# Optimization experiments

Measured on AMD Instinct MI355X. Metric: run time of the kernel, lower is better.

Reference implementation:

```python
import jax, jax.numpy as jnp
import numpy as np

DIM = 1024
HEADS = 16
SCALE = DIM ** (-0.5)  # note: full dim, matching original module


def setup_inputs() -> dict:
    key = jax.random.key(0)
    k1, k2, k3, k4 = jax.random.split(key, 4)
    x = jax.random.normal(k1, (8, 1024, DIM), dtype=jnp.float32)
    w_qkv = jax.random.normal(k2, (DIM, 3 * DIM), dtype=jnp.float32) * (DIM ** -0.5)
    w_out = jax.random.normal(k3, (DIM, DIM), dtype=jnp.float32) * (DIM ** -0.5)
    b_out = jax.random.normal(k4, (DIM,), dtype=jnp.float32) * 0.01
    return {"x": x, "w_qkv": w_qkv, "w_out": w_out, "b_out": b_out}


def reference(x, w_qkv, w_out, b_out):
    b, n, dim = x.shape
    h = HEADS
    d = dim // h
    qkv = x @ w_qkv  # [b, n, 3*dim]
    q, k, v = jnp.split(qkv, 3, axis=-1)
    # 'b n (h d) -> b h n d'
    def to_heads(t):
        return t.reshape(b, n, h, d).transpose(0, 2, 1, 3)
    q, k, v = to_heads(q), to_heads(k), to_heads(v)
    dots = jnp.einsum('bhid,bhjd->bhij', q, k) * SCALE
    attn = jax.nn.softmax(dots, axis=-1)
    out = jnp.einsum('bhij,bhjd->bhid', attn, v)
    out = out.transpose(0, 2, 1, 3).reshape(b, n, dim)  # 'b h n d -> b n (h d)'
    return out @ w_out + b_out  # dropout is identity (rate=0 / eval)
```

## Files before the change

kernel.cpp:

```cpp
#include <hip/hip_runtime.h>

typedef __bf16 bf16x8 __attribute__((ext_vector_type(8)));
typedef __bf16 bf16x4 __attribute__((ext_vector_type(4)));
typedef float  f32x4  __attribute__((ext_vector_type(4)));

#define MFMA16(a, b, c) __builtin_amdgcn_mfma_f32_16x16x32_bf16(a, b, c, 0, 0, 0)
#define GLL(gp, lp) __builtin_amdgcn_global_load_lds( \
    (__attribute__((address_space(1))) void*)(gp),    \
    (__attribute__((address_space(3))) void*)(lp), 16, 0, 0)
#define WAITBAR(N) asm volatile("s_waitcnt vmcnt(" #N ") lgkmcnt(0)\n\ts_barrier" ::: "memory")

__global__ __launch_bounds__(256) void prep_kernel(
    const float* __restrict__ x, __bf16* __restrict__ xb,
    const float* __restrict__ w_qkv, __bf16* __restrict__ wqkvt,
    const float* __restrict__ w_out, __bf16* __restrict__ woutt) {
  __shared__ float tile[64][33];
  const int blk = blockIdx.x;
  const int tid = threadIdx.x;
  if (blk < 1024) {
    const int base = blk * 256 + tid;
#pragma unroll
    for (int it = 0; it < 8; ++it) {
      const int i = base + it * 262144;
      const float4 v = ((const float4*)x)[i];
      bf16x4 o = {(__bf16)v.x, (__bf16)v.y, (__bf16)v.z, (__bf16)v.w};
      ((bf16x4*)xb)[i] = o;
    }
    return;
  }
  const float* in;
  __bf16* out;
  int cols, kt, nt;
  if (blk < 2560) { const int t = blk - 1024; in = w_qkv; out = wqkvt; cols = 3072; kt = t / 96; nt = t - kt * 96; }
  else            { const int t = blk - 2560; in = w_out; out = woutt; cols = 1024; kt = t >> 5; nt = t & 31; }
  const int k0 = kt * 64, n0 = nt * 32;
  const int tx = tid & 31, ty = tid >> 5;
#pragma unroll
  for (int i = 0; i < 64; i += 8)
    tile[ty + i][tx] = in[(k0 + ty + i) * cols + n0 + tx];
  __syncthreads();
  const int c = tid & 63, r0 = tid >> 6;
#pragma unroll
  for (int i = 0; i < 8; ++i) {
    const int r = i * 4 + r0;
    out[(n0 + r) * 1024 + k0 + c] = (__bf16)tile[c][r];
  }
}

#define QSCALE 0.045084220027780106f
__global__ __launch_bounds__(256) void gemm_bt_kernel(
    const __bf16* __restrict__ A, const __bf16* __restrict__ Bt,
    __bf16* __restrict__ qo, __bf16* __restrict__ ko, __bf16* __restrict__ vo) {
  __shared__ __bf16 LDS[3][2][4096];
  const int tid = threadIdx.x;
  const int id = blockIdx.x;
  const int xcd = id & 7, s = id >> 3;
  const int bx = xcd * 3 + s % 3;
  const int by = s / 3;
  const int m0 = by * 128, n0 = bx * 128;
  const int w = tid >> 6, lane = tid & 63;
  const int quad = lane >> 4, l15 = lane & 15;
  const int wm = (w >> 1) * 64, wn = (w & 1) * 64;
  f32x4 acc[4][4] = {};
  const int sr = tid >> 2;
  const int sc = (tid & 3) * 8;
  const __bf16* ag = A + (m0 + sr) * 1024 + sc;
  const __bf16* bg = Bt + (n0 + sr) * 1024 + sc;

  auto stage = [&](int T, int b) {
    const int kk = T * 32;
    GLL(ag + kk,             &LDS[b][0][0] + w * 512);
    GLL(ag + 64 * 1024 + kk, &LDS[b][0][0] + 2048 + w * 512);
    GLL(bg + kk,             &LDS[b][1][0] + w * 512);
    GLL(bg + 64 * 1024 + kk, &LDS[b][1][0] + 2048 + w * 512);
  };
  auto compute = [&](int b) {
    const __bf16* Asb = &LDS[b][0][0];
    const __bf16* Bsb = &LDS[b][1][0];
    bf16x8 af[4], bfr[4];
#pragma unroll
    for (int i = 0; i < 4; ++i)
      af[i] = *(const bf16x8*)(Asb + (wm + i * 16 + l15) * 32 + quad * 8);
#pragma unroll
    for (int j = 0; j < 4; ++j)
      bfr[j] = *(const bf16x8*)(Bsb + (wn + j * 16 + l15) * 32 + quad * 8);
#pragma unroll
    for (int i = 0; i < 4; ++i)
#pragma unroll
      for (int j = 0; j < 4; ++j)
        acc[i][j] = MFMA16(af[i], bfr[j], acc[i][j]);
  };

  stage(0, 0);
  stage(1, 1);
  WAITBAR(4);
  for (int g = 0; g < 10; ++g) {
    const int t = g * 3;
    stage(t + 2, 2); compute(0); WAITBAR(4);
    stage(t + 3, 0); compute(1); WAITBAR(4);
    stage(t + 4, 1); compute(2); WAITBAR(4);
  }
  compute(0);
  asm volatile("s_waitcnt vmcnt(0) lgkmcnt(0)\n\ts_barrier" ::: "memory");
  compute(1);
  __syncthreads();

  const int gcw = n0 + wn;
  float* T = (float*)(&LDS[0][0][0]) + w * 1088;
  const int which = gcw >> 10;
  const int h = (gcw & 1023) >> 6;
  if (which == 2) {
#pragma unroll
    for (int i = 0; i < 4; ++i) {
      int gm = m0 + wm + i * 16 + quad * 4;
      int b = gm >> 10, n = gm & 1023;
      __bf16* vb = vo + ((long)(b * 16 + h) * 64) * 1024 + n;
#pragma unroll
      for (int j = 0; j < 4; ++j) {
        int dd = j * 16 + l15;
        bf16x4 pv = {(__bf16)acc[i][j][0], (__bf16)acc[i][j][1],
                     (__bf16)acc[i][j][2], (__bf16)acc[i][j][3]};
        *(bf16x4*)(vb + (long)dd * 1024) = pv;
      }
    }
  } else {
    __bf16* dst = (which == 0) ? qo : ko;
    const float scl = (which == 0) ? QSCALE : 1.0f;
#pragma unroll
    for (int i = 0; i < 4; ++i) {
#pragma unroll
      for (int j = 0; j < 4; ++j)
#pragma unroll
        for (int r = 0; r < 4; ++r)
          T[(quad * 4 + r) * 68 + j * 16 + l15] = acc[i][j][r];
      const float* Tr = T + l15 * 68 + quad * 16;
      f32x4 c0 = *(const f32x4*)(Tr);
      f32x4 c1 = *(const f32x4*)(Tr + 4);
      f32x4 c2 = *(const f32x4*)(Tr + 8);
      f32x4 c3 = *(const f32x4*)(Tr + 12);
      int gm = m0 + wm + i * 16 + l15;
      int b = gm >> 10, n = gm & 1023;
      __bf16* p = dst + ((long)((b * 16 + h) * 1024 + n)) * 64 + quad * 16;
      bf16x8 o0 = {(__bf16)(c0[0] * scl), (__bf16)(c0[1] * scl),
                   (__bf16)(c0[2] * scl), (__bf16)(c0[3] * scl),
                   (__bf16)(c1[0] * scl), (__bf16)(c1[1] * scl),
                   (__bf16)(c1[2] * scl), (__bf16)(c1[3] * scl)};
      bf16x8 o1 = {(__bf16)(c2[0] * scl), (__bf16)(c2[1] * scl),
                   (__bf16)(c2[2] * scl), (__bf16)(c2[3] * scl),
                   (__bf16)(c3[0] * scl), (__bf16)(c3[1] * scl),
                   (__bf16)(c3[2] * scl), (__bf16)(c3[3] * scl)};
      *(bf16x8*)p = o0;
      *(bf16x8*)(p + 8) = o1;
    }
  }
}

__global__ __launch_bounds__(256) void gemm_out_kernel(
    const __bf16* __restrict__ A, const __bf16* __restrict__ Bt,
    float* __restrict__ outp, const float* __restrict__ bias) {
  __shared__ __bf16 LDS[3][6144];
  const int tid = threadIdx.x;
  const int id = blockIdx.x;
  const int xcd = id & 7, s = id >> 3;
  const int by = xcd * 8 + (s >> 4);
  const int bx = s & 15;
  const int m0 = by * 128, n0 = bx * 64;
  const int w = tid >> 6, lane = tid & 63;
  const int quad = lane >> 4, l15 = lane & 15;
  const int wm = (w >> 1) * 64, wn = (w & 1) * 32;
  f32x4 acc[4][2] = {};
  const int sr = tid >> 2;
  const int sc = (tid & 3) * 8;
  const __bf16* ag = A + (m0 + sr) * 1024 + sc;
  const __bf16* bg = Bt + (n0 + sr) * 1024 + sc;

  auto stage = [&](int T, int b) {
    const int kk = T * 32;
    GLL(ag + kk,             &LDS[b][0] + w * 512);
    GLL(ag + 64 * 1024 + kk, &LDS[b][0] + 2048 + w * 512);
    GLL(bg + kk,             &LDS[b][0] + 4096 + w * 512);
  };
  auto compute = [&](int b) {
    const __bf16* Asb = &LDS[b][0];
    const __bf16* Bsb = &LDS[b][0] + 4096;
    bf16x8 af[4], bfr[2];
#pragma unroll
    for (int i = 0; i < 4; ++i)
      af[i] = *(const bf16x8*)(Asb + (wm + i * 16 + l15) * 32 + quad * 8);
#pragma unroll
    for (int j = 0; j < 2; ++j)
      bfr[j] = *(const bf16x8*)(Bsb + (wn + j * 16 + l15) * 32 + quad * 8);
#pragma unroll
    for (int i = 0; i < 4; ++i)
#pragma unroll
      for (int j = 0; j < 2; ++j)
        acc[i][j] = MFMA16(af[i], bfr[j], acc[i][j]);
  };

  stage(0, 0);
  stage(1, 1);
  WAITBAR(3);
  for (int g = 0; g < 10; ++g) {
    const int t = g * 3;
    stage(t + 2, 2); compute(0); WAITBAR(3);
    stage(t + 3, 0); compute(1); WAITBAR(3);
    stage(t + 4, 1); compute(2); WAITBAR(3);
  }
  compute(0);
  asm volatile("s_waitcnt vmcnt(0) lgkmcnt(0)\n\ts_barrier" ::: "memory");
  compute(1);
  __syncthreads();

  const int cb = n0 + wn;
  float* T = (float*)(&LDS[0][0]) + w * 592;
  f32x4 bv0 = *(const f32x4*)(bias + cb + quad * 8);
  f32x4 bv1 = *(const f32x4*)(bias + cb + quad * 8 + 4);
#pragma unroll
  for (int i = 0; i < 4; ++i) {
#pragma unroll
    for (int j = 0; j < 2; ++j)
#pragma unroll
      for (int r = 0; r < 4; ++r)
        T[(quad * 4 + r) * 36 + j * 16 + l15] = acc[i][j][r];
    const float* Tr = T + l15 * 36 + quad * 8;
    f32x4 v0 = *(const f32x4*)(Tr);
    f32x4 v1 = *(const f32x4*)(Tr + 4);
    v0 += bv0;
    v1 += bv1;
    int gm = m0 + wm + i * 16 + l15;
    float* p = outp + (long)gm * 1024 + cb + quad * 8;
    *(f32x4*)(p) = v0;
    *(f32x4*)(p + 4) = v1;
  }
}

__global__ __launch_bounds__(256, 4) void attn_kernel(
    const __bf16* __restrict__ q, const __bf16* __restrict__ k,
    const __bf16* __restrict__ vt, __bf16* __restrict__ ao) {
  __shared__ __bf16 KV[2][128 * 64];
  __shared__ __bf16 Ps[4][32 * 32];
  __bf16* const Ks = KV[0];
  __bf16* const Vs = KV[1];
  const int tid = threadIdx.x;
  const int bh = blockIdx.x & 127, qt = blockIdx.x >> 7;
  const int w = tid >> 6, lane = tid & 63;
  const int quad = lane >> 4, l15 = lane & 15;
  const int qrow = qt * 128 + w * 32;
  const __bf16* qb = q + (bh * 1024 + qrow) * 64;
  bf16x8 qf[2][2];
#pragma unroll
  for (int f = 0; f < 2; ++f) {
    qf[f][0] = *(const bf16x8*)(qb + (f * 16 + l15) * 64 + quad * 8);
    qf[f][1] = *(const bf16x8*)(qb + (f * 16 + l15) * 64 + 32 + quad * 8);
  }
  f32x4 o[2][4] = {};
  float rs0 = 0.f, rs1 = 0.f;
  const int krow = tid >> 3, kg8 = tid & 7;
  const __bf16* kg = k + (bh * 1024 + krow) * 64 + kg8 * 8;
  const int ksw = (kg8 ^ (krow & 7)) * 8;
  const int vrow = tid >> 2, vg4 = tid & 3;
  const __bf16* vg = vt + (bh * 64 + vrow) * 1024 + vg4 * 8;
  const int kfs0 = (quad ^ (l15 & 7)) * 8;
  const int kfs1 = ((4 + quad) ^ (l15 & 7)) * 8;
  __bf16* const pw = Ps[w];
  const int psw = quad ^ (l15 & 3);

  bf16x8 kvr[4], vvr[4];
#pragma unroll
  for (int p = 0; p < 4; ++p) kvr[p] = *(const bf16x8*)(kg + (p * 32) * 64);
#pragma unroll
  for (int p = 0; p < 4; ++p) vvr[p] = *(const bf16x8*)(vg + p * 32);

  for (int jt = 0; jt < 8; ++jt) {
    __syncthreads();
#pragma unroll
    for (int p = 0; p < 4; ++p)
      *(bf16x8*)(Ks + (krow + p * 32) * 64 + ksw) = kvr[p];
#pragma unroll
    for (int p = 0; p < 4; ++p)
      *(bf16x8*)(Vs + vrow * 128 + (((p * 4 + vg4) ^ (vrow & 15)) * 8)) = vvr[p];
    __syncthreads();
    if (jt < 7) {
      const int j0n = (jt + 1) * 128;
#pragma unroll
      for (int p = 0; p < 4; ++p) kvr[p] = *(const bf16x8*)(kg + (j0n + p * 32) * 64);
#pragma unroll
      for (int p = 0; p < 4; ++p) vvr[p] = *(const bf16x8*)(vg + j0n + p * 32);
    }
#pragma unroll
    for (int Q = 0; Q < 4; ++Q) {
#pragma unroll
      for (int tl = 0; tl < 2; ++tl) {
        const int t = 2 * Q + tl;
        const __bf16* kr = Ks + (t * 16 + l15) * 64;
        bf16x8 kf0 = *(const bf16x8*)(kr + kfs0);
        bf16x8 kf1 = *(const bf16x8*)(kr + kfs1);
        f32x4 z0 = {}, z1 = {};
        __builtin_amdgcn_s_setprio(1);
        z0 = MFMA16(kf0, qf[0][0], z0);
        z0 = MFMA16(kf1, qf[0][1], z0);
        z1 = MFMA16(kf0, qf[1][0], z1);
        z1 = MFMA16(kf1, qf[1][1], z1);
        __builtin_amdgcn_s_setprio(0);
        const float p00 = __builtin_amdgcn_exp2f(z0[0]), p01 = __builtin_amdgcn_exp2f(z0[1]);
        const float p02 = __builtin_amdgcn_exp2f(z0[2]), p03 = __builtin_amdgcn_exp2f(z0[3]);
        const float p10 = __builtin_amdgcn_exp2f(z1[0]), p11 = __builtin_amdgcn_exp2f(z1[1]);
        const float p12 = __builtin_amdgcn_exp2f(z1[2]), p13 = __builtin_amdgcn_exp2f(z1[3]);
        rs0 += (p00 + p01) + (p02 + p03);
        rs1 += (p10 + p11) + (p12 + p13);
        const int g = (2 * tl + (quad >> 1)) ^ (l15 & 3);
        bf16x4 pa = {(__bf16)p00, (__bf16)p01, (__bf16)p02, (__bf16)p03};
        bf16x4 pb = {(__bf16)p10, (__bf16)p11, (__bf16)p12, (__bf16)p13};
        *(bf16x4*)(pw + l15 * 32 + g * 8 + (quad & 1) * 4) = pa;
        *(bf16x4*)(pw + (16 + l15) * 32 + g * 8 + (quad & 1) * 4) = pb;
      }
      bf16x8 pf0 = *(const bf16x8*)(pw + l15 * 32 + psw * 8);
      bf16x8 pf1 = *(const bf16x8*)(pw + (16 + l15) * 32 + psw * 8);
      __builtin_amdgcn_s_setprio(1);
#pragma unroll
      for (int dt = 0; dt < 4; ++dt) {
        bf16x8 vf = *(const bf16x8*)(Vs + (dt * 16 + l15) * 128 + (((Q * 4 + quad) ^ l15) * 8));
        o[0][dt] = MFMA16(pf0, vf, o[0][dt]);
        o[1][dt] = MFMA16(pf1, vf, o[1][dt]);
      }
      __builtin_amdgcn_s_setprio(0);
    }
  }
  rs0 += __shfl_xor(rs0, 16); rs0 += __shfl_xor(rs0, 32);
  rs1 += __shfl_xor(rs1, 16); rs1 += __shfl_xor(rs1, 32);
  __syncthreads();
  float* const T = (float*)KV + w * 1088;
  const int b = bh >> 4, h = bh & 15;
  const int rr = lane >> 3, c8 = lane & 7;
#pragma unroll
  for (int f = 0; f < 2; ++f) {
    const float rsf = f ? rs1 : rs0;
#pragma unroll
    for (int dt = 0; dt < 4; ++dt)
#pragma unroll
      for (int r = 0; r < 4; ++r)
        T[(quad * 4 + r) * 68 + dt * 16 + l15] = o[f][dt][r];
#pragma unroll
    for (int h2 = 0; h2 < 2; ++h2) {
      const int row = h2 * 8 + rr;
      const float inv = 1.0f / __shfl(rsf, row);
      const float* Tr = T + row * 68 + c8 * 8;
      const f32x4 a0 = *(const f32x4*)(Tr);
      const f32x4 a1 = *(const f32x4*)(Tr + 4);
      bf16x8 ov = {(__bf16)(a0[0] * inv), (__bf16)(a0[1] * inv),
                   (__bf16)(a0[2] * inv), (__bf16)(a0[3] * inv),
                   (__bf16)(a1[0] * inv), (__bf16)(a1[1] * inv),
                   (__bf16)(a1[2] * inv), (__bf16)(a1[3] * inv)};
      const long grow = (long)b * 1024 + qrow + f * 16 + row;
      *(bf16x8*)(ao + grow * 1024 + h * 64 + c8 * 8) = ov;
    }
  }
}

extern "C" void kernel_launch(void* const* d_in, const int* in_sizes, int n_in,
                              void* d_out, int out_size, void* d_ws, size_t ws_size,
                              hipStream_t stream) {
  const float* x = (const float*)d_in[0];
  const float* w_qkv = (const float*)d_in[1];
  const float* w_out = (const float*)d_in[2];
  const float* b_out = (const float*)d_in[3];
  float* out = (float*)d_out;

  char* ws = (char*)d_ws;
  __bf16* xb    = (__bf16*)(ws);
  __bf16* wqkvt = (__bf16*)(ws + 16777216);
  __bf16* woutt = (__bf16*)(ws + 23068672);
  __bf16* qw    = (__bf16*)(ws + 25165824);
  __bf16* kw    = (__bf16*)(ws + 41943040);
  __bf16* vw    = (__bf16*)(ws + 58720256);
  __bf16* ao    = xb;

  prep_kernel<<<3072, 256, 0, stream>>>(x, xb, w_qkv, wqkvt, w_out, woutt);
  gemm_bt_kernel<<<1536, 256, 0, stream>>>(xb, wqkvt, qw, kw, vw);
  attn_kernel<<<1024, 256, 0, stream>>>(qw, kw, vw, ao);
  gemm_out_kernel<<<1024, 256, 0, stream>>>(ao, woutt, out, b_out);
}
```

Before: 233.7 us.

## Feed softmax probabilities straight from registers into 16x16x16 MFMA, drop LDS staging

The P·V product now uses the K=16 bf16 MFMA variant, which takes the exp'd score fragments directly in the accumulator layout produced by the QK^T MFMA. This removes the per-wave LDS buffer for P along with its write/read round trip and the associated LDS traffic. In exchange the P·V step issues twice as many MFMAs, each covering half the K depth and possibly at lower throughput, and V fragments are loaded as 4-element reads instead of 8. The exp and row-sum work is unchanged.

```diff
diff --git a/kernel.cpp b/kernel.cpp
--- a/kernel.cpp
+++ b/kernel.cpp
@@ -3,8 +3,10 @@
 typedef __bf16 bf16x8 __attribute__((ext_vector_type(8)));
 typedef __bf16 bf16x4 __attribute__((ext_vector_type(4)));
 typedef float  f32x4  __attribute__((ext_vector_type(4)));
+typedef short  v4s    __attribute__((ext_vector_type(4)));
 
 #define MFMA16(a, b, c) __builtin_amdgcn_mfma_f32_16x16x32_bf16(a, b, c, 0, 0, 0)
+#define MFMA16K16(a, b, c) __builtin_amdgcn_mfma_f32_16x16x16bf16_1k(a, b, c, 0, 0, 0)
 #define GLL(gp, lp) __builtin_amdgcn_global_load_lds( \
     (__attribute__((address_space(1))) void*)(gp),    \
     (__attribute__((address_space(3))) void*)(lp), 16, 0, 0)
@@ -238,7 +240,6 @@
     const __bf16* __restrict__ q, const __bf16* __restrict__ k,
     const __bf16* __restrict__ vt, __bf16* __restrict__ ao) {
   __shared__ __bf16 KV[2][128 * 64];
-  __shared__ __bf16 Ps[4][32 * 32];
   __bf16* const Ks = KV[0];
   __bf16* const Vs = KV[1];
   const int tid = threadIdx.x;
@@ -262,8 +263,8 @@
   const __bf16* vg = vt + (bh * 64 + vrow) * 1024 + vg4 * 8;
   const int kfs0 = (quad ^ (l15 & 7)) * 8;
   const int kfs1 = ((4 + quad) ^ (l15 & 7)) * 8;
-  __bf16* const pw = Ps[w];
-  const int psw = quad ^ (l15 & 3);
+  const int vq2 = quad >> 1;
+  const int vo4 = (quad & 1) * 4;
 
   bf16x8 kvr[4], vvr[4];
 #pragma unroll
@@ -288,40 +289,35 @@
       for (int p = 0; p < 4; ++p) vvr[p] = *(const bf16x8*)(vg + j0n + p * 32);
     }
 #pragma unroll
-    for (int Q = 0; Q < 4; ++Q) {
-#pragma unroll
-      for (int tl = 0; tl < 2; ++tl) {
-        const int t = 2 * Q + tl;
-        const __bf16* kr = Ks + (t * 16 + l15) * 64;
-        bf16x8 kf0 = *(const bf16x8*)(kr + kfs0);
-        bf16x8 kf1 = *(const bf16x8*)(kr + kfs1);
-        f32x4 z0 = {}, z1 = {};
-        __builtin_amdgcn_s_setprio(1);
-        z0 = MFMA16(kf0, qf[0][0], z0);
-        z0 = MFMA16(kf1, qf[0][1], z0);
-        z1 = MFMA16(kf0, qf[1][0], z1);
-        z1 = MFMA16(kf1, qf[1][1], z1);
-        __builtin_amdgcn_s_setprio(0);
-        const float p00 = __builtin_amdgcn_exp2f(z0[0]), p01 = __builtin_amdgcn_exp2f(z0[1]);
-        const float p02 = __builtin_amdgcn_exp2f(z0[2]), p03 = __builtin_amdgcn_exp2f(z0[3]);
-        const float p10 = __builtin_amdgcn_exp2f(z1[0]), p11 = __builtin_amdgcn_exp2f(z1[1]);
-        const float p12 = __builtin_amdgcn_exp2f(z1[2]), p13 = __builtin_amdgcn_exp2f(z1[3]);
-        rs0 += (p00 + p01) + (p02 + p03);
-        rs1 += (p10 + p11) + (p12 + p13);
-        const int g = (2 * tl + (quad >> 1)) ^ (l15 & 3);
-        bf16x4 pa = {(__bf16)p00, (__bf16)p01, (__bf16)p02, (__bf16)p03};
-        bf16x4 pb = {(__bf16)p10, (__bf16)p11, (__bf16)p12, (__bf16)p13};
-        *(bf16x4*)(pw + l15 * 32 + g * 8 + (quad & 1) * 4) = pa;
-        *(bf16x4*)(pw + (16 + l15) * 32 + g * 8 + (quad & 1) * 4) = pb;
-      }
-      bf16x8 pf0 = *(const bf16x8*)(pw + l15 * 32 + psw * 8);
-      bf16x8 pf1 = *(const bf16x8*)(pw + (16 + l15) * 32 + psw * 8);
+    for (int t = 0; t < 8; ++t) {
+      const __bf16* kr = Ks + (t * 16 + l15) * 64;
+      bf16x8 kf0 = *(const bf16x8*)(kr + kfs0);
+      bf16x8 kf1 = *(const bf16x8*)(kr + kfs1);
+      f32x4 z0 = {}, z1 = {};
       __builtin_amdgcn_s_setprio(1);
+      z0 = MFMA16(kf0, qf[0][0], z0);
+      z0 = MFMA16(kf1, qf[0][1], z0);
+      z1 = MFMA16(kf0, qf[1][0], z1);
+      z1 = MFMA16(kf1, qf[1][1], z1);
+      __builtin_amdgcn_s_setprio(0);
+      const float p00 = __builtin_amdgcn_exp2f(z0[0]), p01 = __builtin_amdgcn_exp2f(z0[1]);
+      const float p02 = __builtin_amdgcn_exp2f(z0[2]), p03 = __builtin_amdgcn_exp2f(z0[3]);
+      const float p10 = __builtin_amdgcn_exp2f(z1[0]), p11 = __builtin_amdgcn_exp2f(z1[1]);
+      const float p12 = __builtin_amdgcn_exp2f(z1[2]), p13 = __builtin_amdgcn_exp2f(z1[3]);
+      rs0 += (p00 + p01) + (p02 + p03);
+      rs1 += (p10 + p11) + (p12 + p13);
+      bf16x4 a0 = {(__bf16)p00, (__bf16)p01, (__bf16)p02, (__bf16)p03};
+      bf16x4 a1 = {(__bf16)p10, (__bf16)p11, (__bf16)p12, (__bf16)p13};
+      v4s pa0 = __builtin_bit_cast(v4s, a0);
+      v4s pa1 = __builtin_bit_cast(v4s, a1);
+      const int vgr = 2 * t + vq2;
+      __builtin_amdgcn_s_setprio(1);
 #pragma unroll
       for (int dt = 0; dt < 4; ++dt) {
-        bf16x8 vf = *(const bf16x8*)(Vs + (dt * 16 + l15) * 128 + (((Q * 4 + quad) ^ l15) * 8));
-        o[0][dt] = MFMA16(pf0, vf, o[0][dt]);
-        o[1][dt] = MFMA16(pf1, vf, o[1][dt]);
+        const int dr = dt * 16 + l15;
+        v4s vf = *(const v4s*)(Vs + dr * 128 + (vgr ^ l15) * 8 + vo4);
+        o[0][dt] = MFMA16K16(pa0, vf, o[0][dt]);
+        o[1][dt] = MFMA16K16(pa1, vf, o[1][dt]);
       }
       __builtin_amdgcn_s_setprio(0);
     }
```

New measurement: 491.3 us. +110.2%, slower.
